# Kernel tuning notes

Hardware: AMD Instinct MI355X
Metric: run time of the kernel (lower is better)

## Reference

```python
import jax, jax.numpy as jnp
import numpy as np
from jax import lax

B, C_IN, C_OUT, H, W, K, MID = 16, 256, 256, 64, 64, 3, 64
BN_EPS = 1e-5


def setup_inputs() -> dict:
    key = jax.random.key(0)
    ks = jax.random.split(key, 16)
    inp = {
        'x': jax.random.normal(ks[0], (B, C_IN, H, W), dtype=jnp.float32),
        # 4 kernel banks: (4, c2, c1//g, k, k)
        'weight': jax.random.normal(ks[1], (4, C_OUT, C_IN, K, K), dtype=jnp.float32) * 0.05,
        'gamma': jnp.ones((C_OUT,), jnp.float32),
        'beta': jnp.zeros((C_OUT,), jnp.float32),
    }
    # four attention branches: Linear(c, mid, bias=False) -> ReLU -> Linear(mid, 4, bias=True)
    names = ['s', 'c', 'f', 'w']
    for i, n in enumerate(names):
        inp[f'fc_{n}_w1'] = jax.random.normal(ks[2 + 3 * i], (MID, C_IN), dtype=jnp.float32) * 0.05
        inp[f'fc_{n}_w2'] = jax.random.normal(ks[3 + 3 * i], (4, MID), dtype=jnp.float32) * 0.05
        inp[f'fc_{n}_b2'] = jax.random.normal(ks[4 + 3 * i], (4,), dtype=jnp.float32) * 0.05
    return inp


def _branch(pooled, w1, w2, b2):
    # pooled: [B, C]; w1: [MID, C]; w2: [4, MID]
    h = jax.nn.relu(pooled @ w1.T)
    return jax.nn.softmax(h @ w2.T + b2, axis=1)  # [B, 4]


def reference(x, weight, gamma, beta,
              fc_s_w1, fc_s_w2, fc_s_b2,
              fc_c_w1, fc_c_w2, fc_c_b2,
              fc_f_w1, fc_f_w2, fc_f_b2,
              fc_w_w1, fc_w_w2, fc_w_b2):
    b = x.shape[0]
    pooled = jnp.mean(x, axis=(2, 3))  # GAP -> [B, C]
    alpha = (_branch(pooled, fc_s_w1, fc_s_w2, fc_s_b2)
             * _branch(pooled, fc_c_w1, fc_c_w2, fc_c_b2)
             * _branch(pooled, fc_f_w1, fc_f_w2, fc_f_b2)
             * _branch(pooled, fc_w_w1, fc_w_w2, fc_w_b2))  # [B, 4]
    # per-sample dynamic kernels: [B, out_c, in_c, k, k]
    dyn_w = jnp.einsum('bn,noikl->boikl', alpha, weight)

    def conv_one(xi, wi):
        # xi: [C, H, W]; wi: [out_c, in_c, k, k]
        return lax.conv_general_dilated(
            xi[None], wi, window_strides=(1, 1), padding='SAME',
            dimension_numbers=('NCHW', 'OIHW', 'NCHW'))[0]

    out = jax.vmap(conv_one)(x, dyn_w)  # [B, out_c, H, W]

    # BatchNorm2d (training-mode batch statistics)
    mean = jnp.mean(out, axis=(0, 2, 3))
    var = jnp.var(out, axis=(0, 2, 3))
    out = (out - mean[None, :, None, None]) * jax.lax.rsqrt(var + BN_EPS)[None, :, None, None]
    return out * gamma[None, :, None, None] + beta[None, :, None, None]
```

## Files before the change

### kernel.cpp

```cpp
#include <hip/hip_runtime.h>
#include <math.h>

#define BB 16
#define CIN 256
#define COUT 256
#define HH 64
#define WW 64
#define NBANK_STRIDE 589824

typedef short bf16x8 __attribute__((ext_vector_type(8)));
typedef float f32x4 __attribute__((ext_vector_type(4)));

#define WS_XT_OFF 32768
#define WS_DW_OFF 33587200
#define WS_NEED   52461568ULL

static __device__ __forceinline__ unsigned short f2bf(float f) {
    union { float f; unsigned u; } v; v.f = f;
    unsigned r = v.u + 0x7FFF + ((v.u >> 16) & 1);
    return (unsigned short)(r >> 16);
}

struct AttnParams {
    const float* w1[4];
    const float* w2[4];
    const float* b2[4];
};

__global__ __launch_bounds__(256) void gap_kernel(const float* __restrict__ x,
                                                  float* __restrict__ pooled) {
    const int plane = blockIdx.x;
    const float4* p = (const float4*)(x + (size_t)plane * 4096);
    const int t = threadIdx.x;
    float s = 0.f;
#pragma unroll
    for (int i = 0; i < 4; ++i) {
        float4 v = p[t + 256 * i];
        s += v.x + v.y + v.z + v.w;
    }
#pragma unroll
    for (int off = 32; off > 0; off >>= 1) s += __shfl_down(s, off, 64);
    __shared__ float red[4];
    if ((t & 63) == 0) red[t >> 6] = s;
    __syncthreads();
    if (t == 0) pooled[plane] = (red[0] + red[1] + red[2] + red[3]) * (1.0f / 4096.0f);
}

__global__ __launch_bounds__(64) void attn_kernel(const float* __restrict__ pooled,
                                                  AttnParams p,
                                                  float* __restrict__ alpha) {
    const int b = blockIdx.x;
    const int t = threadIdx.x;
    __shared__ float ps[256];
    __shared__ float hs[64];
    __shared__ float lg[4];
    __shared__ float prod[4];
#pragma unroll
    for (int i = 0; i < 4; ++i) ps[t + 64 * i] = pooled[b * 256 + t + 64 * i];
    if (t < 4) prod[t] = 1.f;
    __syncthreads();
    for (int n = 0; n < 4; ++n) {
        const float* w1 = p.w1[n];
        float h = 0.f;
        for (int c = 0; c < 256; ++c) h += w1[t * 256 + c] * ps[c];
        hs[t] = fmaxf(h, 0.f);
        __syncthreads();
        if (t < 4) {
            const float* w2 = p.w2[n];
            float l = p.b2[n][t];
            for (int m = 0; m < 64; ++m) l += w2[t * 64 + m] * hs[m];
            lg[t] = l;
        }
        __syncthreads();
        if (t == 0) {
            float mx = fmaxf(fmaxf(lg[0], lg[1]), fmaxf(lg[2], lg[3]));
            float e0 = expf(lg[0] - mx), e1 = expf(lg[1] - mx);
            float e2 = expf(lg[2] - mx), e3 = expf(lg[3] - mx);
            float inv = 1.f / (e0 + e1 + e2 + e3);
            prod[0] *= e0 * inv;
            prod[1] *= e1 * inv;
            prod[2] *= e2 * inv;
            prod[3] *= e3 * inv;
        }
        __syncthreads();
    }
    if (t < 4) alpha[b * 4 + t] = prod[t];
}

__global__ __launch_bounds__(256) void xpose_kernel(const float* __restrict__ x,
                                                    unsigned short* __restrict__ xT) {
    const int ci0 = blockIdx.x * 32;
    const int h = blockIdx.y;
    const int b = blockIdx.z;
    const int t = threadIdx.x;
    __shared__ __align__(16) unsigned short tile[64][40];
    {
        const int ci = t >> 3;
        const int l = t & 7;
        const float4* src = (const float4*)(x + ((size_t)(b * 256 + ci0 + ci)) * 4096 + h * 64);
        float4 v1 = src[l * 2];
        float4 v2 = src[l * 2 + 1];
        tile[l * 8 + 0][ci] = f2bf(v1.x);
        tile[l * 8 + 1][ci] = f2bf(v1.y);
        tile[l * 8 + 2][ci] = f2bf(v1.z);
        tile[l * 8 + 3][ci] = f2bf(v1.w);
        tile[l * 8 + 4][ci] = f2bf(v2.x);
        tile[l * 8 + 5][ci] = f2bf(v2.y);
        tile[l * 8 + 6][ci] = f2bf(v2.z);
        tile[l * 8 + 7][ci] = f2bf(v2.w);
    }
    __syncthreads();
    {
        const int w = t >> 2;
        const int s = t & 3;
        bf16x8 val = *(const bf16x8*)&tile[w][s * 8];
        *(bf16x8*)&xT[((size_t)b * 4096 + h * 64 + w) * 256 + ci0 + s * 8] = val;
    }
}

__global__ __launch_bounds__(256) void dynw_kernel(const float* __restrict__ wt,
                                                   const float* __restrict__ alpha,
                                                   unsigned short* __restrict__ dynwT) {
    const int co = blockIdx.x;
    const int ci = threadIdx.x;
    float w[4][9];
#pragma unroll
    for (int n = 0; n < 4; ++n) {
        const size_t base = ((size_t)(n * 256 + co) * 256 + ci) * 9;
#pragma unroll
        for (int k = 0; k < 9; ++k) w[n][k] = wt[base + k];
    }
    for (int b = 0; b < BB; ++b) {
        const float a0 = alpha[b * 4 + 0];
        const float a1 = alpha[b * 4 + 1];
        const float a2 = alpha[b * 4 + 2];
        const float a3 = alpha[b * 4 + 3];
#pragma unroll
        for (int k = 0; k < 9; ++k) {
            float v = a0 * w[0][k] + a1 * w[1][k] + a2 * w[2][k] + a3 * w[3][k];
            dynwT[((size_t)(b * 9 + k) * 256 + co) * 256 + ci] = f2bf(v);
        }
    }
}

__global__ __launch_bounds__(256) void conv_mfma_kernel(const unsigned short* __restrict__ xT,
                                                        const unsigned short* __restrict__ dynwT,
                                                        float* __restrict__ out) {
    const int nt = blockIdx.x;
    const int mt = blockIdx.y;
    const int b = blockIdx.z;
    const int t = threadIdx.x;
    const int lane = t & 63;
    const int wv = t >> 6;
    const int wx = wv & 1;
    const int wy = wv >> 1;
    const int mh = lane & 15;
    const int q = lane >> 4;
    const int r0 = nt * 2;
    const int co0 = mt * 128;

    __shared__ __align__(16) short xs[264 * 40];
    __shared__ __align__(16) short As[128 * 40];

    f32x4 acc[4][4];
#pragma unroll
    for (int i = 0; i < 4; ++i)
#pragma unroll
        for (int j = 0; j < 4; ++j) acc[i][j] = (f32x4){0.f, 0.f, 0.f, 0.f};

    const int a_base = (wy * 64 + mh) * 40 + q * 8;
    const bf16x8 zero8 = {0, 0, 0, 0, 0, 0, 0, 0};

    for (int cc = 0; cc < 8; ++cc) {
        const int ci0 = cc * 32;
        __syncthreads();
#pragma unroll
        for (int i = 0; i < 5; ++i) {
            int idx = t + 256 * i;
            if (idx < 1056) {
                int p = idx >> 2;
                int sub = idx & 3;
                int lr = p / 66;
                int lc = p - lr * 66;
                int r = r0 - 1 + lr;
                int c = lc - 1;
                bf16x8 v = zero8;
                if ((unsigned)r < 64u && (unsigned)c < 64u)
                    v = *(const bf16x8*)&xT[((size_t)b * 4096 + r * 64 + c) * 256 + ci0 + sub * 8];
                *(bf16x8*)&xs[p * 40 + sub * 8] = v;
            }
        }
        for (int khw = 0; khw < 9; ++khw) {
            const int kh = khw / 3;
            const int kw = khw - kh * 3;
            if (khw) __syncthreads();
#pragma unroll
            for (int i = 0; i < 2; ++i) {
                int e = t * 2 + i;
                int row = e >> 2;
                int sub = e & 3;
                bf16x8 v = *(const bf16x8*)&dynwT[((size_t)(b * 9 + khw) * 256 + co0 + row) * 256 + ci0 + sub * 8];
                *(bf16x8*)&As[row * 40 + sub * 8] = v;
            }
            __syncthreads();
            const int boff = ((wx + kh) * 66 + kw + mh) * 40 + q * 8;
            bf16x8 bf[4], af[4];
#pragma unroll
            for (int ni = 0; ni < 4; ++ni) bf[ni] = *(const bf16x8*)&xs[boff + ni * 640];
#pragma unroll
            for (int mi = 0; mi < 4; ++mi) af[mi] = *(const bf16x8*)&As[a_base + mi * 640];
#pragma unroll
            for (int mi = 0; mi < 4; ++mi)
#pragma unroll
                for (int ni = 0; ni < 4; ++ni)
                    acc[mi][ni] = __builtin_amdgcn_mfma_f32_16x16x32_bf16(af[mi], bf[ni], acc[mi][ni], 0, 0, 0);
        }
    }
    const int h = r0 + wx;
#pragma unroll
    for (int mi = 0; mi < 4; ++mi) {
#pragma unroll
        for (int ni = 0; ni < 4; ++ni) {
            const int w = ni * 16 + mh;
#pragma unroll
            for (int reg = 0; reg < 4; ++reg) {
                const int co = co0 + wy * 64 + mi * 16 + q * 4 + reg;
                out[(((size_t)b * 256 + co) << 12) + (h << 6) + w] = acc[mi][ni][reg];
            }
        }
    }
}

__global__ __launch_bounds__(256) void conv_fp32_kernel(const float* __restrict__ x,
                                                        const float* __restrict__ wt,
                                                        const float* __restrict__ alpha,
                                                        float* __restrict__ out) {
    const int h = blockIdx.x;
    const int cot = blockIdx.y;
    const int b = blockIdx.z;
    const int t = threadIdx.x;
    const int tx = t & 15;
    const int ty = t >> 4;
    const int co0 = cot * 64;

    __shared__ __align__(16) float xsf[32][68];
    __shared__ __align__(16) float wshf[3][32][68];

    const float a0 = alpha[b * 4 + 0];
    const float a1 = alpha[b * 4 + 1];
    const float a2 = alpha[b * 4 + 2];
    const float a3 = alpha[b * 4 + 3];

    float acc[4][4];
#pragma unroll
    for (int i = 0; i < 4; ++i)
#pragma unroll
        for (int j = 0; j < 4; ++j) acc[i][j] = 0.f;

    const size_t xbase = (size_t)b * CIN * 4096;

    for (int kh = 0; kh < 3; ++kh) {
        const int r = h + kh - 1;
        if (r < 0 || r >= HH) continue;
        for (int chunk = 0; chunk < 8; ++chunk) {
            const int ci0 = chunk * 32;
            __syncthreads();
#pragma unroll
            for (int i = 0; i < 8; ++i) {
                int flat = t + 256 * i;
                int ci = flat >> 6;
                int w = flat & 63;
                xsf[ci][1 + w] = x[xbase + (size_t)(ci0 + ci) * 4096 + r * 64 + w];
            }
            if (t < 32) {
                xsf[t][0] = 0.f;
                xsf[t][65] = 0.f;
                xsf[t][66] = 0.f;
                xsf[t][67] = 0.f;
            }
#pragma unroll
            for (int j = 0; j < 24; ++j) {
                int e = t + 256 * j;
                int co = e / 96;
                int rem = e - co * 96;
                int ci = rem / 3;
                int kw = rem - ci * 3;
                size_t g = (((size_t)(co0 + co) * 256 + (ci0 + ci)) * 3 + kh) * 3 + kw;
                float v = a0 * wt[g] + a1 * wt[g + NBANK_STRIDE] +
                          a2 * wt[g + 2 * NBANK_STRIDE] + a3 * wt[g + 3 * NBANK_STRIDE];
                wshf[kw][ci][co] = v;
            }
            __syncthreads();
            for (int ci = 0; ci < 32; ++ci) {
                float4 w0 = *(const float4*)&wshf[0][ci][tx * 4];
                float4 w1v = *(const float4*)&wshf[1][ci][tx * 4];
                float4 w2v = *(const float4*)&wshf[2][ci][tx * 4];
                float4 xa = *(const float4*)&xsf[ci][ty * 4];
                float4 xb = *(const float4*)&xsf[ci][ty * 4 + 4];
                float v[8] = {xa.x, xa.y, xa.z, xa.w, xb.x, xb.y, xb.z, xb.w};
                float aw[3][4] = {{w0.x, w0.y, w0.z, w0.w},
                                  {w1v.x, w1v.y, w1v.z, w1v.w},
                                  {w2v.x, w2v.y, w2v.z, w2v.w}};
#pragma unroll
                for (int kw = 0; kw < 3; ++kw)
#pragma unroll
                    for (int i = 0; i < 4; ++i)
#pragma unroll
                        for (int j = 0; j < 4; ++j)
                            acc[i][j] += aw[kw][i] * v[j + kw];
            }
        }
    }
    size_t obase = (((size_t)b * COUT + co0 + tx * 4) * 64 + h) * 64 + ty * 4;
#pragma unroll
    for (int i = 0; i < 4; ++i) {
        float4 o = {acc[i][0], acc[i][1], acc[i][2], acc[i][3]};
        *(float4*)&out[obase + (size_t)i * 4096] = o;
    }
}

__global__ __launch_bounds__(256) void bn_stats_kernel(const float* __restrict__ out,
                                                       const float* __restrict__ gamma,
                                                       const float* __restrict__ beta,
                                                       float* __restrict__ scale,
                                                       float* __restrict__ shift) {
    const int co = blockIdx.x;
    const int t = threadIdx.x;
    float s = 0.f, sq = 0.f;
    for (int b = 0; b < BB; ++b) {
        const float4* p = (const float4*)(out + ((size_t)b * 256 + co) * 4096);
#pragma unroll
        for (int i = 0; i < 4; ++i) {
            float4 v = p[t + 256 * i];
            s += v.x + v.y + v.z + v.w;
            sq += v.x * v.x + v.y * v.y + v.z * v.z + v.w * v.w;
        }
    }
#pragma unroll
    for (int off = 32; off > 0; off >>= 1) {
        s += __shfl_down(s, off, 64);
        sq += __shfl_down(sq, off, 64);
    }
    __shared__ float rs[4], rq[4];
    if ((t & 63) == 0) {
        rs[t >> 6] = s;
        rq[t >> 6] = sq;
    }
    __syncthreads();
    if (t == 0) {
        float S = rs[0] + rs[1] + rs[2] + rs[3];
        float Q = rq[0] + rq[1] + rq[2] + rq[3];
        float mean = S * (1.f / 65536.f);
        float var = Q * (1.f / 65536.f) - mean * mean;
        float inv = rsqrtf(var + 1e-5f);
        float sc = gamma[co] * inv;
        scale[co] = sc;
        shift[co] = beta[co] - mean * sc;
    }
}

__global__ __launch_bounds__(256) void bn_apply_kernel(float* __restrict__ out,
                                                       const float* __restrict__ scale,
                                                       const float* __restrict__ shift) {
    const int gid = blockIdx.x * 256 + threadIdx.x;
    const int c = (gid >> 10) & 255;
    float4* p = (float4*)out;
    float4 v = p[gid];
    const float sc = scale[c], sh = shift[c];
    v.x = v.x * sc + sh;
    v.y = v.y * sc + sh;
    v.z = v.z * sc + sh;
    v.w = v.w * sc + sh;
    p[gid] = v;
}

extern "C" void kernel_launch(void* const* d_in, const int* in_sizes, int n_in,
                              void* d_out, int out_size, void* d_ws, size_t ws_size,
                              hipStream_t stream) {
    (void)in_sizes; (void)n_in; (void)out_size;
    const float* x = (const float*)d_in[0];
    const float* wt = (const float*)d_in[1];
    const float* gamma = (const float*)d_in[2];
    const float* beta = (const float*)d_in[3];
    AttnParams ap;
    for (int n = 0; n < 4; ++n) {
        ap.w1[n] = (const float*)d_in[4 + 3 * n];
        ap.w2[n] = (const float*)d_in[5 + 3 * n];
        ap.b2[n] = (const float*)d_in[6 + 3 * n];
    }
    float* ws = (float*)d_ws;
    float* pooled = ws;
    float* alpha = ws + 4096;
    float* scale = ws + 4160;
    float* shift = ws + 4416;
    float* out = (float*)d_out;

    gap_kernel<<<4096, 256, 0, stream>>>(x, pooled);
    attn_kernel<<<16, 64, 0, stream>>>(pooled, ap, alpha);

    if (ws_size >= WS_NEED) {
        unsigned short* xT = (unsigned short*)((char*)d_ws + WS_XT_OFF);
        unsigned short* dynwT = (unsigned short*)((char*)d_ws + WS_DW_OFF);
        xpose_kernel<<<dim3(8, 64, 16), 256, 0, stream>>>(x, xT);
        dynw_kernel<<<256, 256, 0, stream>>>(wt, alpha, dynwT);
        conv_mfma_kernel<<<dim3(32, 2, 16), 256, 0, stream>>>(xT, dynwT, out);
    } else {
        conv_fp32_kernel<<<dim3(64, 4, 16), 256, 0, stream>>>(x, wt, alpha, out);
    }

    bn_stats_kernel<<<256, 256, 0, stream>>>(out, gamma, beta, scale, shift);
    bn_apply_kernel<<<16384, 256, 0, stream>>>(out, scale, shift);
}
```

Before: 335.6 us.

## Fuse GAP into transpose, BN stats into conv epilogue, enlarge and double-buffer conv tile

Global average pooling moves into the transpose kernel, which accumulates per-channel sums with atomics into a zeroed workspace. The attention MLP now runs its four branches in parallel across wavefronts. The MFMA conv tile grows to 4 rows with 8 N-fragments per wave. Weight tiles are double-buffered in LDS with register prefetch, and per-block BN partial sums are produced in the epilogue. This removes the separate GAP pass and the full BN stats read of the output, at the cost of higher register pressure, fewer blocks, and atomic float ordering.

```diff
diff --git a/kernel.cpp b/kernel.cpp
--- a/kernel.cpp
+++ b/kernel.cpp
@@ -15,10 +15,10 @@
 #define WS_DW_OFF 33587200
 #define WS_NEED   52461568ULL
 
-static __device__ __forceinline__ unsigned short f2bf(float f) {
+static __device__ __forceinline__ short f2bf(float f) {
     union { float f; unsigned u; } v; v.f = f;
     unsigned r = v.u + 0x7FFF + ((v.u >> 16) & 1);
-    return (unsigned short)(r >> 16);
+    return (short)(r >> 16);
 }
 
 struct AttnParams {
@@ -27,73 +27,18 @@
     const float* b2[4];
 };
 
-__global__ __launch_bounds__(256) void gap_kernel(const float* __restrict__ x,
-                                                  float* __restrict__ pooled) {
-    const int plane = blockIdx.x;
-    const float4* p = (const float4*)(x + (size_t)plane * 4096);
-    const int t = threadIdx.x;
-    float s = 0.f;
-#pragma unroll
-    for (int i = 0; i < 4; ++i) {
-        float4 v = p[t + 256 * i];
-        s += v.x + v.y + v.z + v.w;
-    }
-#pragma unroll
-    for (int off = 32; off > 0; off >>= 1) s += __shfl_down(s, off, 64);
-    __shared__ float red[4];
-    if ((t & 63) == 0) red[t >> 6] = s;
-    __syncthreads();
-    if (t == 0) pooled[plane] = (red[0] + red[1] + red[2] + red[3]) * (1.0f / 4096.0f);
-}
-
-__global__ __launch_bounds__(64) void attn_kernel(const float* __restrict__ pooled,
-                                                  AttnParams p,
-                                                  float* __restrict__ alpha) {
-    const int b = blockIdx.x;
-    const int t = threadIdx.x;
-    __shared__ float ps[256];
-    __shared__ float hs[64];
-    __shared__ float lg[4];
-    __shared__ float prod[4];
-#pragma unroll
-    for (int i = 0; i < 4; ++i) ps[t + 64 * i] = pooled[b * 256 + t + 64 * i];
-    if (t < 4) prod[t] = 1.f;
-    __syncthreads();
-    for (int n = 0; n < 4; ++n) {
-        const float* w1 = p.w1[n];
-        float h = 0.f;
-        for (int c = 0; c < 256; ++c) h += w1[t * 256 + c] * ps[c];
-        hs[t] = fmaxf(h, 0.f);
-        __syncthreads();
-        if (t < 4) {
-            const float* w2 = p.w2[n];
-            float l = p.b2[n][t];
-            for (int m = 0; m < 64; ++m) l += w2[t * 64 + m] * hs[m];
-            lg[t] = l;
-        }
-        __syncthreads();
-        if (t == 0) {
-            float mx = fmaxf(fmaxf(lg[0], lg[1]), fmaxf(lg[2], lg[3]));
-            float e0 = expf(lg[0] - mx), e1 = expf(lg[1] - mx);
-            float e2 = expf(lg[2] - mx), e3 = expf(lg[3] - mx);
-            float inv = 1.f / (e0 + e1 + e2 + e3);
-            prod[0] *= e0 * inv;
-            prod[1] *= e1 * inv;
-            prod[2] *= e2 * inv;
-            prod[3] *= e3 * inv;
-        }
-        __syncthreads();
-    }
-    if (t < 4) alpha[b * 4 + t] = prod[t];
+__global__ __launch_bounds__(256) void zero_kernel(float* __restrict__ ws) {
+    ws[blockIdx.x * 256 + threadIdx.x] = 0.f;
 }
 
 __global__ __launch_bounds__(256) void xpose_kernel(const float* __restrict__ x,
-                                                    unsigned short* __restrict__ xT) {
+                                                    short* __restrict__ xT,
+                                                    float* __restrict__ pooled) {
     const int ci0 = blockIdx.x * 32;
     const int h = blockIdx.y;
     const int b = blockIdx.z;
     const int t = threadIdx.x;
-    __shared__ __align__(16) unsigned short tile[64][40];
+    __shared__ __align__(16) short tile[64][40];
     {
         const int ci = t >> 3;
         const int l = t & 7;
@@ -108,6 +53,11 @@
         tile[l * 8 + 5][ci] = f2bf(v2.y);
         tile[l * 8 + 6][ci] = f2bf(v2.z);
         tile[l * 8 + 7][ci] = f2bf(v2.w);
+        float s = v1.x + v1.y + v1.z + v1.w + v2.x + v2.y + v2.z + v2.w;
+        s += __shfl_xor(s, 1, 64);
+        s += __shfl_xor(s, 2, 64);
+        s += __shfl_xor(s, 4, 64);
+        if (l == 0) atomicAdd(&pooled[b * 256 + ci0 + ci], s);
     }
     __syncthreads();
     {
@@ -118,9 +68,53 @@
     }
 }
 
+__global__ __launch_bounds__(256) void attn_kernel(AttnParams p, float* __restrict__ ws_f) {
+    const int b = blockIdx.x;
+    const int t = threadIdx.x;
+    const int wv = t >> 6;
+    const int lane = t & 63;
+    __shared__ float ps[256];
+    __shared__ float hs[4][64];
+    __shared__ float lg[4][4];
+    __shared__ float sm[4][4];
+    ws_f[4096 + b * 256 + t] = 0.f;
+    ps[t] = ws_f[b * 256 + t] * (1.0f / 4096.0f);
+    __syncthreads();
+    {
+        const float4* w1v = (const float4*)(p.w1[wv] + lane * 256);
+        float h = 0.f;
+#pragma unroll 8
+        for (int i = 0; i < 64; ++i) {
+            float4 w4 = w1v[i];
+            h += w4.x * ps[i * 4 + 0] + w4.y * ps[i * 4 + 1] +
+                 w4.z * ps[i * 4 + 2] + w4.w * ps[i * 4 + 3];
+        }
+        hs[wv][lane] = fmaxf(h, 0.f);
+    }
+    __syncthreads();
+    if (t < 16) {
+        const int n = t >> 2, j = t & 3;
+        const float* w2 = p.w2[n];
+        float l = p.b2[n][j];
+        for (int m = 0; m < 64; ++m) l += w2[j * 64 + m] * hs[n][m];
+        lg[n][j] = l;
+    }
+    __syncthreads();
+    if (t < 4) {
+        const int n = t;
+        float mx = fmaxf(fmaxf(lg[n][0], lg[n][1]), fmaxf(lg[n][2], lg[n][3]));
+        float e0 = expf(lg[n][0] - mx), e1 = expf(lg[n][1] - mx);
+        float e2 = expf(lg[n][2] - mx), e3 = expf(lg[n][3] - mx);
+        float inv = 1.f / (e0 + e1 + e2 + e3);
+        sm[n][0] = e0 * inv; sm[n][1] = e1 * inv; sm[n][2] = e2 * inv; sm[n][3] = e3 * inv;
+    }
+    __syncthreads();
+    if (t < 4) ws_f[b * 256 + t] = sm[0][t] * sm[1][t] * sm[2][t] * sm[3][t];
+}
+
 __global__ __launch_bounds__(256) void dynw_kernel(const float* __restrict__ wt,
-                                                   const float* __restrict__ alpha,
-                                                   unsigned short* __restrict__ dynwT) {
+                                                   const float* __restrict__ ws_f,
+                                                   short* __restrict__ dynwT) {
     const int co = blockIdx.x;
     const int ci = threadIdx.x;
     float w[4][9];
@@ -131,10 +125,10 @@
         for (int k = 0; k < 9; ++k) w[n][k] = wt[base + k];
     }
     for (int b = 0; b < BB; ++b) {
-        const float a0 = alpha[b * 4 + 0];
-        const float a1 = alpha[b * 4 + 1];
-        const float a2 = alpha[b * 4 + 2];
-        const float a3 = alpha[b * 4 + 3];
+        const float a0 = ws_f[b * 256 + 0];
+        const float a1 = ws_f[b * 256 + 1];
+        const float a2 = ws_f[b * 256 + 2];
+        const float a3 = ws_f[b * 256 + 3];
 #pragma unroll
         for (int k = 0; k < 9; ++k) {
             float v = a0 * w[0][k] + a1 * w[1][k] + a2 * w[2][k] + a3 * w[3][k];
@@ -143,9 +137,10 @@
     }
 }
 
-__global__ __launch_bounds__(256) void conv_mfma_kernel(const unsigned short* __restrict__ xT,
-                                                        const unsigned short* __restrict__ dynwT,
-                                                        float* __restrict__ out) {
+__global__ __launch_bounds__(256, 2) void conv_mfma_kernel(const short* __restrict__ xT,
+                                                           const short* __restrict__ dynwT,
+                                                           float* __restrict__ out,
+                                                           float* __restrict__ bn_part) {
     const int nt = blockIdx.x;
     const int mt = blockIdx.y;
     const int b = blockIdx.z;
@@ -156,28 +151,37 @@
     const int wy = wv >> 1;
     const int mh = lane & 15;
     const int q = lane >> 4;
-    const int r0 = nt * 2;
+    const int r0 = nt * 4;
     const int co0 = mt * 128;
 
-    __shared__ __align__(16) short xs[264 * 40];
-    __shared__ __align__(16) short As[128 * 40];
-
-    f32x4 acc[4][4];
+    __shared__ __align__(16) short xs[396 * 40];
+    __shared__ __align__(16) short As[2][128 * 40];
+    __shared__ float red[128][2][2];
+
+    f32x4 acc[4][8];
 #pragma unroll
     for (int i = 0; i < 4; ++i)
 #pragma unroll
-        for (int j = 0; j < 4; ++j) acc[i][j] = (f32x4){0.f, 0.f, 0.f, 0.f};
-
-    const int a_base = (wy * 64 + mh) * 40 + q * 8;
+        for (int j = 0; j < 8; ++j) acc[i][j] = (f32x4){0.f, 0.f, 0.f, 0.f};
+
+    const int arow0 = t >> 2;
+    const int asub = t & 3;
+    const short* Ab = dynwT + (size_t)b * 9 * 65536 + (co0 + arow0) * 256 + asub * 8;
+    const int a_lds0 = arow0 * 40 + asub * 8;
+    const int a_lds1 = (arow0 + 64) * 40 + asub * 8;
+    const int a_rd = (wy * 64 + mh) * 40 + q * 8;
+
     const bf16x8 zero8 = {0, 0, 0, 0, 0, 0, 0, 0};
 
     for (int cc = 0; cc < 8; ++cc) {
         const int ci0 = cc * 32;
         __syncthreads();
-#pragma unroll
-        for (int i = 0; i < 5; ++i) {
+        bf16x8 pa0 = *(const bf16x8*)(Ab + ci0);
+        bf16x8 pa1 = *(const bf16x8*)(Ab + 64 * 256 + ci0);
+#pragma unroll
+        for (int i = 0; i < 7; ++i) {
             int idx = t + 256 * i;
-            if (idx < 1056) {
+            if (idx < 1584) {
                 int p = idx >> 2;
                 int sub = idx & 3;
                 int lr = p / 66;
@@ -190,173 +194,105 @@
                 *(bf16x8*)&xs[p * 40 + sub * 8] = v;
             }
         }
+        *(bf16x8*)&As[0][a_lds0] = pa0;
+        *(bf16x8*)&As[0][a_lds1] = pa1;
+        __syncthreads();
+#pragma unroll
         for (int khw = 0; khw < 9; ++khw) {
             const int kh = khw / 3;
             const int kw = khw - kh * 3;
-            if (khw) __syncthreads();
-#pragma unroll
-            for (int i = 0; i < 2; ++i) {
-                int e = t * 2 + i;
-                int row = e >> 2;
-                int sub = e & 3;
-                bf16x8 v = *(const bf16x8*)&dynwT[((size_t)(b * 9 + khw) * 256 + co0 + row) * 256 + ci0 + sub * 8];
-                *(bf16x8*)&As[row * 40 + sub * 8] = v;
+            bf16x8 na0, na1;
+            if (khw < 8) {
+                na0 = *(const bf16x8*)(Ab + (khw + 1) * 65536 + ci0);
+                na1 = *(const bf16x8*)(Ab + (khw + 1) * 65536 + 64 * 256 + ci0);
+            }
+            bf16x8 bfr[8];
+#pragma unroll
+            for (int ni = 0; ni < 8; ++ni) {
+                const int row_l = wx * 2 + (ni >> 2) + kh;
+                const int col_l = (ni & 3) * 16 + kw + mh;
+                bfr[ni] = *(const bf16x8*)&xs[(row_l * 66 + col_l) * 40 + q * 8];
+            }
+#pragma unroll
+            for (int mi = 0; mi < 4; ++mi) {
+                bf16x8 af = *(const bf16x8*)&As[khw & 1][a_rd + mi * 640];
+#pragma unroll
+                for (int ni = 0; ni < 8; ++ni)
+                    acc[mi][ni] = __builtin_amdgcn_mfma_f32_16x16x32_bf16(af, bfr[ni], acc[mi][ni], 0, 0, 0);
+            }
+            if (khw < 8) {
+                *(bf16x8*)&As[(khw + 1) & 1][a_lds0] = na0;
+                *(bf16x8*)&As[(khw + 1) & 1][a_lds1] = na1;
             }
             __syncthreads();
-            const int boff = ((wx + kh) * 66 + kw + mh) * 40 + q * 8;
-            bf16x8 bf[4], af[4];
-#pragma unroll
-            for (int ni = 0; ni < 4; ++ni) bf[ni] = *(const bf16x8*)&xs[boff + ni * 640];
-#pragma unroll
-            for (int mi = 0; mi < 4; ++mi) af[mi] = *(const bf16x8*)&As[a_base + mi * 640];
-#pragma unroll
-            for (int mi = 0; mi < 4; ++mi)
-#pragma unroll
-                for (int ni = 0; ni < 4; ++ni)
-                    acc[mi][ni] = __builtin_amdgcn_mfma_f32_16x16x32_bf16(af[mi], bf[ni], acc[mi][ni], 0, 0, 0);
-        }
-    }
-    const int h = r0 + wx;
+        }
+    }
+
+    float s16[4][4], q16[4][4];
+#pragma unroll
+    for (int mi = 0; mi < 4; ++mi)
+#pragma unroll
+        for (int reg = 0; reg < 4; ++reg) { s16[mi][reg] = 0.f; q16[mi][reg] = 0.f; }
+
 #pragma unroll
     for (int mi = 0; mi < 4; ++mi) {
 #pragma unroll
-        for (int ni = 0; ni < 4; ++ni) {
-            const int w = ni * 16 + mh;
+        for (int ni = 0; ni < 8; ++ni) {
+            const int pix = wx * 128 + ni * 16 + mh;
+            const int h = r0 + (pix >> 6);
+            const int w = pix & 63;
 #pragma unroll
             for (int reg = 0; reg < 4; ++reg) {
                 const int co = co0 + wy * 64 + mi * 16 + q * 4 + reg;
-                out[(((size_t)b * 256 + co) << 12) + (h << 6) + w] = acc[mi][ni][reg];
-            }
-        }
-    }
-}
-
-__global__ __launch_bounds__(256) void conv_fp32_kernel(const float* __restrict__ x,
-                                                        const float* __restrict__ wt,
-                                                        const float* __restrict__ alpha,
-                                                        float* __restrict__ out) {
-    const int h = blockIdx.x;
-    const int cot = blockIdx.y;
-    const int b = blockIdx.z;
-    const int t = threadIdx.x;
-    const int tx = t & 15;
-    const int ty = t >> 4;
-    const int co0 = cot * 64;
-
-    __shared__ __align__(16) float xsf[32][68];
-    __shared__ __align__(16) float wshf[3][32][68];
-
-    const float a0 = alpha[b * 4 + 0];
-    const float a1 = alpha[b * 4 + 1];
-    const float a2 = alpha[b * 4 + 2];
-    const float a3 = alpha[b * 4 + 3];
-
-    float acc[4][4];
-#pragma unroll
-    for (int i = 0; i < 4; ++i)
-#pragma unroll
-        for (int j = 0; j < 4; ++j) acc[i][j] = 0.f;
-
-    const size_t xbase = (size_t)b * CIN * 4096;
-
-    for (int kh = 0; kh < 3; ++kh) {
-        const int r = h + kh - 1;
-        if (r < 0 || r >= HH) continue;
-        for (int chunk = 0; chunk < 8; ++chunk) {
-            const int ci0 = chunk * 32;
-            __syncthreads();
-#pragma unroll
-            for (int i = 0; i < 8; ++i) {
-                int flat = t + 256 * i;
-                int ci = flat >> 6;
-                int w = flat & 63;
-                xsf[ci][1 + w] = x[xbase + (size_t)(ci0 + ci) * 4096 + r * 64 + w];
-            }
-            if (t < 32) {
-                xsf[t][0] = 0.f;
-                xsf[t][65] = 0.f;
-                xsf[t][66] = 0.f;
-                xsf[t][67] = 0.f;
-            }
-#pragma unroll
-            for (int j = 0; j < 24; ++j) {
-                int e = t + 256 * j;
-                int co = e / 96;
-                int rem = e - co * 96;
-                int ci = rem / 3;
-                int kw = rem - ci * 3;
-                size_t g = (((size_t)(co0 + co) * 256 + (ci0 + ci)) * 3 + kh) * 3 + kw;
-                float v = a0 * wt[g] + a1 * wt[g + NBANK_STRIDE] +
-                          a2 * wt[g + 2 * NBANK_STRIDE] + a3 * wt[g + 3 * NBANK_STRIDE];
-                wshf[kw][ci][co] = v;
-            }
-            __syncthreads();
-            for (int ci = 0; ci < 32; ++ci) {
-                float4 w0 = *(const float4*)&wshf[0][ci][tx * 4];
-                float4 w1v = *(const float4*)&wshf[1][ci][tx * 4];
-                float4 w2v = *(const float4*)&wshf[2][ci][tx * 4];
-                float4 xa = *(const float4*)&xsf[ci][ty * 4];
-                float4 xb = *(const float4*)&xsf[ci][ty * 4 + 4];
-                float v[8] = {xa.x, xa.y, xa.z, xa.w, xb.x, xb.y, xb.z, xb.w};
-                float aw[3][4] = {{w0.x, w0.y, w0.z, w0.w},
-                                  {w1v.x, w1v.y, w1v.z, w1v.w},
-                                  {w2v.x, w2v.y, w2v.z, w2v.w}};
-#pragma unroll
-                for (int kw = 0; kw < 3; ++kw)
-#pragma unroll
-                    for (int i = 0; i < 4; ++i)
-#pragma unroll
-                        for (int j = 0; j < 4; ++j)
-                            acc[i][j] += aw[kw][i] * v[j + kw];
-            }
-        }
-    }
-    size_t obase = (((size_t)b * COUT + co0 + tx * 4) * 64 + h) * 64 + ty * 4;
-#pragma unroll
-    for (int i = 0; i < 4; ++i) {
-        float4 o = {acc[i][0], acc[i][1], acc[i][2], acc[i][3]};
-        *(float4*)&out[obase + (size_t)i * 4096] = o;
-    }
-}
-
-__global__ __launch_bounds__(256) void bn_stats_kernel(const float* __restrict__ out,
-                                                       const float* __restrict__ gamma,
-                                                       const float* __restrict__ beta,
-                                                       float* __restrict__ scale,
-                                                       float* __restrict__ shift) {
-    const int co = blockIdx.x;
-    const int t = threadIdx.x;
-    float s = 0.f, sq = 0.f;
-    for (int b = 0; b < BB; ++b) {
-        const float4* p = (const float4*)(out + ((size_t)b * 256 + co) * 4096);
-#pragma unroll
-        for (int i = 0; i < 4; ++i) {
-            float4 v = p[t + 256 * i];
-            s += v.x + v.y + v.z + v.w;
-            sq += v.x * v.x + v.y * v.y + v.z * v.z + v.w * v.w;
-        }
-    }
-#pragma unroll
-    for (int off = 32; off > 0; off >>= 1) {
-        s += __shfl_down(s, off, 64);
-        sq += __shfl_down(sq, off, 64);
-    }
-    __shared__ float rs[4], rq[4];
-    if ((t & 63) == 0) {
-        rs[t >> 6] = s;
-        rq[t >> 6] = sq;
-    }
-    __syncthreads();
-    if (t == 0) {
-        float S = rs[0] + rs[1] + rs[2] + rs[3];
-        float Q = rq[0] + rq[1] + rq[2] + rq[3];
-        float mean = S * (1.f / 65536.f);
-        float var = Q * (1.f / 65536.f) - mean * mean;
-        float inv = rsqrtf(var + 1e-5f);
-        float sc = gamma[co] * inv;
-        scale[co] = sc;
-        shift[co] = beta[co] - mean * sc;
-    }
+                const float e = acc[mi][ni][reg];
+                out[(((size_t)b * 256 + co) << 12) + (h << 6) + w] = e;
+                s16[mi][reg] += e;
+                q16[mi][reg] += e * e;
+            }
+        }
+    }
+#pragma unroll
+    for (int mi = 0; mi < 4; ++mi)
+#pragma unroll
+        for (int reg = 0; reg < 4; ++reg) {
+            float s = s16[mi][reg], sq = q16[mi][reg];
+            s += __shfl_xor(s, 1, 64);  sq += __shfl_xor(sq, 1, 64);
+            s += __shfl_xor(s, 2, 64);  sq += __shfl_xor(sq, 2, 64);
+            s += __shfl_xor(s, 4, 64);  sq += __shfl_xor(sq, 4, 64);
+            s += __shfl_xor(s, 8, 64);  sq += __shfl_xor(sq, 8, 64);
+            if (mh == 0) {
+                const int co_l = wy * 64 + mi * 16 + q * 4 + reg;
+                red[co_l][0][wx] = s;
+                red[co_l][1][wx] = sq;
+            }
+        }
+    __syncthreads();
+    {
+        const int co_l = t >> 1;
+        const int st = t & 1;
+        float v = red[co_l][st][0] + red[co_l][st][1];
+        atomicAdd(&bn_part[(st * 256 + co0 + co_l) * 8 + (nt & 7)], v);
+    }
+}
+
+__global__ __launch_bounds__(256) void bn_finalize_kernel(const float* __restrict__ bn_part,
+                                                          const float* __restrict__ gamma,
+                                                          const float* __restrict__ beta,
+                                                          float* __restrict__ scale,
+                                                          float* __restrict__ shift) {
+    const int co = threadIdx.x;
+    float S = 0.f, Q = 0.f;
+#pragma unroll
+    for (int s = 0; s < 8; ++s) {
+        S += bn_part[(co) * 8 + s];
+        Q += bn_part[(256 + co) * 8 + s];
+    }
+    const float mean = S * (1.f / 65536.f);
+    const float var = Q * (1.f / 65536.f) - mean * mean;
+    const float inv = rsqrtf(var + 1e-5f);
+    const float sc = gamma[co] * inv;
+    scale[co] = sc;
+    shift[co] = beta[co] - mean * sc;
 }
 
 __global__ __launch_bounds__(256) void bn_apply_kernel(float* __restrict__ out,
@@ -374,6 +310,176 @@
     p[gid] = v;
 }
 
+__global__ __launch_bounds__(256) void gap_kernel(const float* __restrict__ x,
+                                                  float* __restrict__ pooled) {
+    const int plane = blockIdx.x;
+    const float4* p = (const float4*)(x + (size_t)plane * 4096);
+    const int t = threadIdx.x;
+    float s = 0.f;
+#pragma unroll
+    for (int i = 0; i < 4; ++i) {
+        float4 v = p[t + 256 * i];
+        s += v.x + v.y + v.z + v.w;
+    }
+#pragma unroll
+    for (int off = 32; off > 0; off >>= 1) s += __shfl_down(s, off, 64);
+    __shared__ float red[4];
+    if ((t & 63) == 0) red[t >> 6] = s;
+    __syncthreads();
+    if (t == 0) pooled[plane] = (red[0] + red[1] + red[2] + red[3]) * (1.0f / 4096.0f);
+}
+
+__global__ __launch_bounds__(64) void attn64_kernel(const float* __restrict__ pooled,
+                                                    AttnParams p,
+                                                    float* __restrict__ alpha) {
+    const int b = blockIdx.x;
+    const int t = threadIdx.x;
+    __shared__ float ps[256];
+    __shared__ float hs[64];
+    __shared__ float lg[4];
+    __shared__ float prod[4];
+#pragma unroll
+    for (int i = 0; i < 4; ++i) ps[t + 64 * i] = pooled[b * 256 + t + 64 * i];
+    if (t < 4) prod[t] = 1.f;
+    __syncthreads();
+    for (int n = 0; n < 4; ++n) {
+        const float* w1 = p.w1[n];
+        float h = 0.f;
+        for (int c = 0; c < 256; ++c) h += w1[t * 256 + c] * ps[c];
+        hs[t] = fmaxf(h, 0.f);
+        __syncthreads();
+        if (t < 4) {
+            const float* w2 = p.w2[n];
+            float l = p.b2[n][t];
+            for (int m = 0; m < 64; ++m) l += w2[t * 64 + m] * hs[m];
+            lg[t] = l;
+        }
+        __syncthreads();
+        if (t == 0) {
+            float mx = fmaxf(fmaxf(lg[0], lg[1]), fmaxf(lg[2], lg[3]));
+            float e0 = expf(lg[0] - mx), e1 = expf(lg[1] - mx);
+            float e2 = expf(lg[2] - mx), e3 = expf(lg[3] - mx);
+            float inv = 1.f / (e0 + e1 + e2 + e3);
+            prod[0] *= e0 * inv; prod[1] *= e1 * inv;
+            prod[2] *= e2 * inv; prod[3] *= e3 * inv;
+        }
+        __syncthreads();
+    }
+    if (t < 4) alpha[b * 4 + t] = prod[t];
+}
+
+__global__ __launch_bounds__(256) void conv_fp32_kernel(const float* __restrict__ x,
+                                                        const float* __restrict__ wt,
+                                                        const float* __restrict__ alpha,
+                                                        float* __restrict__ out) {
+    const int h = blockIdx.x;
+    const int cot = blockIdx.y;
+    const int b = blockIdx.z;
+    const int t = threadIdx.x;
+    const int tx = t & 15;
+    const int ty = t >> 4;
+    const int co0 = cot * 64;
+    __shared__ __align__(16) float xsf[32][68];
+    __shared__ __align__(16) float wshf[3][32][68];
+    const float a0 = alpha[b * 4 + 0], a1 = alpha[b * 4 + 1];
+    const float a2 = alpha[b * 4 + 2], a3 = alpha[b * 4 + 3];
+    float acc[4][4];
+#pragma unroll
+    for (int i = 0; i < 4; ++i)
+#pragma unroll
+        for (int j = 0; j < 4; ++j) acc[i][j] = 0.f;
+    const size_t xbase = (size_t)b * CIN * 4096;
+    for (int kh = 0; kh < 3; ++kh) {
+        const int r = h + kh - 1;
+        if (r < 0 || r >= HH) continue;
+        for (int chunk = 0; chunk < 8; ++chunk) {
+            const int ci0 = chunk * 32;
+            __syncthreads();
+#pragma unroll
+            for (int i = 0; i < 8; ++i) {
+                int flat = t + 256 * i;
+                int ci = flat >> 6;
+                int w = flat & 63;
+                xsf[ci][1 + w] = x[xbase + (size_t)(ci0 + ci) * 4096 + r * 64 + w];
+            }
+            if (t < 32) { xsf[t][0] = 0.f; xsf[t][65] = 0.f; xsf[t][66] = 0.f; xsf[t][67] = 0.f; }
+#pragma unroll
+            for (int j = 0; j < 24; ++j) {
+                int e = t + 256 * j;
+                int co = e / 96;
+                int rem = e - co * 96;
+                int ci = rem / 3;
+                int kw = rem - ci * 3;
+                size_t g = (((size_t)(co0 + co) * 256 + (ci0 + ci)) * 3 + kh) * 3 + kw;
+                wshf[kw][ci][co] = a0 * wt[g] + a1 * wt[g + NBANK_STRIDE] +
+                                   a2 * wt[g + 2 * NBANK_STRIDE] + a3 * wt[g + 3 * NBANK_STRIDE];
+            }
+            __syncthreads();
+            for (int ci = 0; ci < 32; ++ci) {
+                float4 w0 = *(const float4*)&wshf[0][ci][tx * 4];
+                float4 w1v = *(const float4*)&wshf[1][ci][tx * 4];
+                float4 w2v = *(const float4*)&wshf[2][ci][tx * 4];
+                float4 xa = *(const float4*)&xsf[ci][ty * 4];
+                float4 xb = *(const float4*)&xsf[ci][ty * 4 + 4];
+                float v[8] = {xa.x, xa.y, xa.z, xa.w, xb.x, xb.y, xb.z, xb.w};
+                float aw[3][4] = {{w0.x, w0.y, w0.z, w0.w},
+                                  {w1v.x, w1v.y, w1v.z, w1v.w},
+                                  {w2v.x, w2v.y, w2v.z, w2v.w}};
+#pragma unroll
+                for (int kw = 0; kw < 3; ++kw)
+#pragma unroll
+                    for (int i = 0; i < 4; ++i)
+#pragma unroll
+                        for (int j = 0; j < 4; ++j)
+                            acc[i][j] += aw[kw][i] * v[j + kw];
+            }
+        }
+    }
+    size_t obase = (((size_t)b * COUT + co0 + tx * 4) * 64 + h) * 64 + ty * 4;
+#pragma unroll
+    for (int i = 0; i < 4; ++i) {
+        float4 o = {acc[i][0], acc[i][1], acc[i][2], acc[i][3]};
+        *(float4*)&out[obase + (size_t)i * 4096] = o;
+    }
+}
+
+__global__ __launch_bounds__(256) void bn_stats_kernel(const float* __restrict__ out,
+                                                       const float* __restrict__ gamma,
+                                                       const float* __restrict__ beta,
+                                                       float* __restrict__ scale,
+                                                       float* __restrict__ shift) {
+    const int co = blockIdx.x;
+    const int t = threadIdx.x;
+    float s = 0.f, sq = 0.f;
+    for (int b = 0; b < BB; ++b) {
+        const float4* p = (const float4*)(out + ((size_t)b * 256 + co) * 4096);
+#pragma unroll
+        for (int i = 0; i < 4; ++i) {
+            float4 v = p[t + 256 * i];
+            s += v.x + v.y + v.z + v.w;
+            sq += v.x * v.x + v.y * v.y + v.z * v.z + v.w * v.w;
+        }
+    }
+#pragma unroll
+    for (int off = 32; off > 0; off >>= 1) {
+        s += __shfl_down(s, off, 64);
+        sq += __shfl_down(sq, off, 64);
+    }
+    __shared__ float rs[4], rq[4];
+    if ((t & 63) == 0) { rs[t >> 6] = s; rq[t >> 6] = sq; }
+    __syncthreads();
+    if (t == 0) {
+        float S = rs[0] + rs[1] + rs[2] + rs[3];
+        float Q = rq[0] + rq[1] + rq[2] + rq[3];
+        float mean = S * (1.f / 65536.f);
+        float var = Q * (1.f / 65536.f) - mean * mean;
+        float inv = rsqrtf(var + 1e-5f);
+        float sc = gamma[co] * inv;
+        scale[co] = sc;
+        shift[co] = beta[co] - mean * sc;
+    }
+}
+
 extern "C" void kernel_launch(void* const* d_in, const int* in_sizes, int n_in,
                               void* d_out, int out_size, void* d_ws, size_t ws_size,
                               hipStream_t stream) {
@@ -388,26 +494,32 @@
         ap.w2[n] = (const float*)d_in[5 + 3 * n];
         ap.b2[n] = (const float*)d_in[6 + 3 * n];
     }
-    float* ws = (float*)d_ws;
-    float* pooled = ws;
-    float* alpha = ws + 4096;
-    float* scale = ws + 4160;
-    float* shift = ws + 4416;
+    float* ws_f = (float*)d_ws;
     float* out = (float*)d_out;
 
-    gap_kernel<<<4096, 256, 0, stream>>>(x, pooled);
-    attn_kernel<<<16, 64, 0, stream>>>(pooled, ap, alpha);
-
     if (ws_size >= WS_NEED) {
-        unsigned short* xT = (unsigned short*)((char*)d_ws + WS_XT_OFF);
-        unsigned short* dynwT = (unsigned short*)((char*)d_ws + WS_DW_OFF);
-        xpose_kernel<<<dim3(8, 64, 16), 256, 0, stream>>>(x, xT);
-        dynw_kernel<<<256, 256, 0, stream>>>(wt, alpha, dynwT);
-        conv_mfma_kernel<<<dim3(32, 2, 16), 256, 0, stream>>>(xT, dynwT, out);
+        short* xT = (short*)((char*)d_ws + WS_XT_OFF);
+        short* dynwT = (short*)((char*)d_ws + WS_DW_OFF);
+        float* bn_part = ws_f + 4096;
+        float* scale = ws_f;
+        float* shift = ws_f + 256;
+
+        zero_kernel<<<16, 256, 0, stream>>>(ws_f);
+        xpose_kernel<<<dim3(8, 64, 16), 256, 0, stream>>>(x, xT, ws_f);
+        attn_kernel<<<16, 256, 0, stream>>>(ap, ws_f);
+        dynw_kernel<<<256, 256, 0, stream>>>(wt, ws_f, dynwT);
+        conv_mfma_kernel<<<dim3(16, 2, 16), 256, 0, stream>>>(xT, dynwT, out, bn_part);
+        bn_finalize_kernel<<<1, 256, 0, stream>>>(bn_part, gamma, beta, scale, shift);
+        bn_apply_kernel<<<16384, 256, 0, stream>>>(out, scale, shift);
     } else {
+        float* pooled = ws_f;
+        float* alpha = ws_f + 4096;
+        float* scale = ws_f + 4160;
+        float* shift = ws_f + 4416;
+        gap_kernel<<<4096, 256, 0, stream>>>(x, pooled);
+        attn64_kernel<<<16, 64, 0, stream>>>(pooled, ap, alpha);
         conv_fp32_kernel<<<dim3(64, 4, 16), 256, 0, stream>>>(x, wt, alpha, out);
-    }
-
-    bn_stats_kernel<<<256, 256, 0, stream>>>(out, gamma, beta, scale, shift);
-    bn_apply_kernel<<<16384, 256, 0, stream>>>(out, scale, shift);
-}
+        bn_stats_kernel<<<256, 256, 0, stream>>>(out, gamma, beta, scale, shift);
+        bn_apply_kernel<<<16384, 256, 0, stream>>>(out, scale, shift);
+    }
+}
```

Result: faster. 277.8 us (-17.2%).
